# Performance work log

Hardware: AMD Instinct MI355X
Metric: run time of the kernel (lower is better)

The kernel has to match this reference:

```python
import jax, jax.numpy as jnp
import numpy as np

B, S, D, H, DH, RANK = 1, 2048, 1024, 16, 64, 16
NUM_ITERS = 5
EPS = 1e-6


def setup_inputs() -> dict:
    ks = jax.random.split(jax.random.key(0), 8)
    scale = 1.0 / np.sqrt(D)
    return {
        "x": jax.random.normal(ks[0], (B, S, D), dtype=jnp.float32),
        "Wq": jax.random.normal(ks[1], (D, D), dtype=jnp.float32) * scale,
        "Wk": jax.random.normal(ks[2], (D, D), dtype=jnp.float32) * scale,
        "Wv": jax.random.normal(ks[3], (D, D), dtype=jnp.float32) * scale,
        "Wo": jax.random.normal(ks[4], (D, D), dtype=jnp.float32) * scale,
        "bandwidth": jnp.array(1.0, dtype=jnp.float32),
        "diag_scale": jnp.ones((1, H, 1), dtype=jnp.float32),
        "pos_embedding": jax.random.normal(ks[5], (2048, RANK), dtype=jnp.float32) * 0.02,
        "head_proj": jax.random.normal(ks[6], (H, RANK, RANK), dtype=jnp.float32) * 0.02,
        "reg": jnp.array(0.1, dtype=jnp.float32),
        "lambda_reg": jnp.array(0.1, dtype=jnp.float32),
    }


def reference(x, Wq, Wk, Wv, Wo, bandwidth, diag_scale, pos_embedding, head_proj, reg, lambda_reg):
    b, s, d = x.shape
    h, dh = H, DH

    def heads(t):  # (b,s,d) -> (b,h,s,dh)
        return t.reshape(b, s, h, dh).transpose(0, 2, 1, 3)

    q = heads(x @ Wq)
    k = heads(x @ Wk)
    v = heads(x @ Wv)

    # RBF kernel via norm trick: ||q-k||^2 = ||q||^2 + ||k||^2 - 2 q.k
    bw = jax.nn.softplus(bandwidth) + EPS
    q_nsq = jnp.sum(q * q, axis=-1, keepdims=True)            # (b,h,s,1)
    k_nsq = jnp.sum(k * k, axis=-1, keepdims=True)            # (b,h,s,1)
    dist_sq = q_nsq + jnp.swapaxes(k_nsq, -2, -1) - 2.0 * jnp.einsum('bhsd,bhtd->bhst', q, k)
    dist_sq = jnp.maximum(dist_sq, 0.0)
    K = jnp.exp(-dist_sq / (2.0 * bw * bw))                   # (b,h,s,s)

    lam = jax.nn.softplus(lambda_reg)

    # Preconditioner P = diag(d) + U U^T
    kdiag = jnp.diagonal(K, axis1=-2, axis2=-1)               # (b,h,s)
    diag_p = jax.nn.softplus(kdiag) * diag_scale + reg        # (b,h,s)
    U = jnp.einsum('sr,hrp->hsp', pos_embedding[:s], head_proj)  # (h,s,rank)

    # Preconditioned Richardson iteration for (K + lam I) alpha = V
    alpha = jnp.zeros_like(v)
    for _ in range(NUM_ITERS):
        r = v - (jnp.einsum('bhst,bhtd->bhsd', K, alpha) + lam * alpha)
        ut_r = jnp.einsum('htr,bhtd->bhrd', U, r)
        p = r * diag_p[..., None] + jnp.einsum('hsr,bhrd->bhsd', U, ut_r)
        alpha = alpha + p

    out = jnp.einsum('bhst,bhtd->bhsd', K, alpha)             # output = K alpha
    out = out.transpose(0, 2, 1, 3).reshape(b, s, d) @ Wo
    return out
```

## Files before the change

### kernel.cpp

```cpp
#include <hip/hip_runtime.h>
#include <cstdint>
#include <cstddef>

constexpr int kS  = 2048;
constexpr int kD  = 1024;
constexpr int kH  = 16;
constexpr int kDH = 64;
constexpr int kR  = 16;

typedef __attribute__((ext_vector_type(8))) short bf16x8;
typedef __attribute__((ext_vector_type(4))) float f32x4;

__device__ __forceinline__ unsigned short kar_f2bf(float x) {
  unsigned u = __float_as_uint(x);
  return (unsigned short)((u + 0x7FFFu + ((u >> 16) & 1u)) >> 16);
}
__device__ __forceinline__ float kar_bf2f(short h) {
  return __uint_as_float((unsigned)(unsigned short)h << 16);
}
__device__ __forceinline__ void kar_split_bf(float x, short& hi, short& lo) {
  unsigned short h = kar_f2bf(x);
  float hf = __uint_as_float((unsigned)h << 16);
  hi = (short)h;
  lo = (short)kar_f2bf(x - hf);
}

__global__ __launch_bounds__(64) void kar_scalars_kernel(const float* __restrict__ bw,
                                                         const float* __restrict__ lreg,
                                                         double* __restrict__ SC) {
  if (threadIdx.x == 0) {
    double b = log1p(exp((double)bw[0])) + 1e-6;
    SC[0] = 1.0 / (2.0 * b * b);
    SC[1] = log1p(exp((double)lreg[0]));
  }
}

__global__ __launch_bounds__(256) void kar_u_kernel(const float* __restrict__ pe,
                                                    const float* __restrict__ hp,
                                                    float* __restrict__ U) {
  int o = blockIdx.x * 256 + threadIdx.x;
  int r = o & 15, s = (o >> 4) & 2047, h = o >> 15;
  double acc = 0.0;
#pragma unroll
  for (int rp = 0; rp < kR; rp++)
    acc += (double)pe[s * kR + rp] * (double)hp[((h * kR) + rp) * kR + r];
  U[o] = (float)acc;
}

__global__ __launch_bounds__(256) void kar_utr_partial_kernel(
    const float* __restrict__ Ubuf, const float* __restrict__ rbuf,
    double* __restrict__ utrp) {
  const int h  = blockIdx.y;
  const int sb = blockIdx.x * 64;
  const int t  = threadIdx.x;
  __shared__ float Uch[32][16];
  __shared__ float Rch[32][64];
  double acc[4] = {};
  for (int cs = 0; cs < 64; cs += 32) {
    __syncthreads();
    if (t < 128) {
      const int i = t >> 2, f = (t & 3) * 4;
      *(float4*)&Uch[i][f] = *(const float4*)&Ubuf[((size_t)(h * kS) + sb + cs + i) * kR + f];
    }
#pragma unroll
    for (int rep = 0; rep < 2; rep++) {
      const int e = t + rep * 256;
      const int i = e >> 4, c = (e & 15) * 4;
      *(float4*)&Rch[i][c] = *(const float4*)&rbuf[((size_t)(h * kS) + sb + cs + i) * kDH + c];
    }
    __syncthreads();
    for (int i = 0; i < 32; i++) {
#pragma unroll
      for (int rep = 0; rep < 4; rep++) {
        const int p = t + rep * 256;
        const int r = p >> 6, d = p & 63;
        acc[rep] += (double)Uch[i][r] * (double)Rch[i][d];
      }
    }
  }
#pragma unroll
  for (int rep = 0; rep < 4; rep++) {
    const int p = t + rep * 256;
    const int r = p >> 6, d = p & 63;
    utrp[(((size_t)(h * 32) + blockIdx.x) * kR + r) * kDH + d] = acc[rep];
  }
}

__global__ __launch_bounds__(256) void kar_utr_reduce_kernel(const double* __restrict__ utrp,
                                                             double* __restrict__ utr) {
  int o = blockIdx.x * 256 + threadIdx.x;
  int h = o >> 10, rd = o & 1023;
  double s = 0.0;
#pragma unroll
  for (int j = 0; j < 32; j++) s += utrp[(size_t)h * 32768 + (size_t)j * 1024 + rd];
  utr[o] = s;
}

__global__ __launch_bounds__(256) void kar_update_kernel(
    const float* __restrict__ rsrc, const double* __restrict__ dgp,
    const float* __restrict__ Ubuf, const double* __restrict__ utr,
    float* __restrict__ alpha, int first) {
  int e = blockIdx.x * 256 + threadIdx.x;
  const int d = e & 63;
  const int s = (e >> 6) & 2047;
  const int h = e >> 17;
  const double rv = (double)rsrc[e];
  const double dp = dgp[h * kS + s];
  const float*  Us = &Ubuf[((size_t)(h * kS) + s) * kR];
  const double* uh = &utr[(size_t)h * kR * kDH];
  double sum = 0.0;
#pragma unroll
  for (int ri = 0; ri < kR; ri++) sum += (double)Us[ri] * uh[ri * kDH + d];
  const double p = rv * dp + sum;
  const double an = (first ? 0.0 : (double)alpha[e]) + p;
  alpha[e] = (float)an;
}

__global__ __launch_bounds__(256) void kar_update_t_kernel(
    const float* __restrict__ rsrc, const double* __restrict__ dgp,
    const float* __restrict__ Ubuf, const double* __restrict__ utr,
    float* __restrict__ alpha, short* __restrict__ ath, int first) {
  const int h = blockIdx.y, s0 = blockIdx.x * 64;
  __shared__ float T[64][65];
  const int t = threadIdx.x;
  const int r16 = t >> 4, c4 = (t & 15) * 4;
  const double* uh = &utr[(size_t)h * kR * kDH];
#pragma unroll
  for (int it = 0; it < 4; it++) {
    const int row = it * 16 + r16;
    const int s = s0 + row;
    const size_t eg = ((size_t)h * kS + s) * kDH + c4;
    const float4 rv4 = *(const float4*)&rsrc[eg];
    const double dp = dgp[h * kS + s];
    const float* Us = &Ubuf[((size_t)h * kS + s) * kR];
    double sum0 = 0.0, sum1 = 0.0, sum2 = 0.0, sum3 = 0.0;
#pragma unroll
    for (int ri = 0; ri < kR; ri++) {
      const double u = (double)Us[ri];
      const double* ur = &uh[ri * kDH + c4];
      sum0 += u * ur[0]; sum1 += u * ur[1];
      sum2 += u * ur[2]; sum3 += u * ur[3];
    }
    double a0 = (first ? 0.0 : (double)alpha[eg + 0]) + ((double)rv4.x * dp + sum0);
    double a1 = (first ? 0.0 : (double)alpha[eg + 1]) + ((double)rv4.y * dp + sum1);
    double a2 = (first ? 0.0 : (double)alpha[eg + 2]) + ((double)rv4.z * dp + sum2);
    double a3 = (first ? 0.0 : (double)alpha[eg + 3]) + ((double)rv4.w * dp + sum3);
    float4 o;
    o.x = (float)a0; o.y = (float)a1; o.z = (float)a2; o.w = (float)a3;
    *(float4*)&alpha[eg] = o;
    T[row][c4] = o.x; T[row][c4 + 1] = o.y; T[row][c4 + 2] = o.z; T[row][c4 + 3] = o.w;
  }
  __syncthreads();
#pragma unroll
  for (int it = 0; it < 4; it++) {
    int d = it * 16 + r16;
    float v0 = T[c4][d], v1 = T[c4 + 1][d], v2 = T[c4 + 2][d], v3 = T[c4 + 3][d];
    *(short4*)&ath[((size_t)h * kDH + d) * kS + s0 + c4] =
        make_short4((short)kar_f2bf(v0), (short)kar_f2bf(v1),
                    (short)kar_f2bf(v2), (short)kar_f2bf(v3));
  }
}


__global__ __launch_bounds__(256) void kar_xsplit_kernel(const float* __restrict__ x,
                                                         short* __restrict__ xh,
                                                         short* __restrict__ xl) {
  size_t e = ((size_t)blockIdx.x * 256 + threadIdx.x) * 4;
  float4 a = *(const float4*)&x[e];
  short h0, l0, h1, l1, h2, l2, h3, l3;
  kar_split_bf(a.x, h0, l0); kar_split_bf(a.y, h1, l1);
  kar_split_bf(a.z, h2, l2); kar_split_bf(a.w, h3, l3);
  *(short4*)&xh[e] = make_short4(h0, h1, h2, h3);
  *(short4*)&xl[e] = make_short4(l0, l1, l2, l3);
}

__global__ __launch_bounds__(256) void kar_wsplit_kernel(
    const float* __restrict__ Wq, const float* __restrict__ Wk,
    const float* __restrict__ Wv, const float* __restrict__ Wo,
    short* __restrict__ WTh, short* __restrict__ WTl) {
  const float* W = (blockIdx.z == 0) ? Wq : (blockIdx.z == 1) ? Wk
                 : (blockIdx.z == 2) ? Wv : Wo;
  short* oh = WTh + (size_t)blockIdx.z * kD * kD;
  short* ol = WTl + (size_t)blockIdx.z * kD * kD;
  const int n0 = blockIdx.x * 64, k0 = blockIdx.y * 64;
  __shared__ float T[64][65];
  const int t = threadIdx.x;
  const int r16 = t >> 4, c4 = (t & 15) * 4;
#pragma unroll
  for (int it = 0; it < 4; it++) {
    int r = it * 16 + r16;
    float4 a = *(const float4*)&W[(size_t)(k0 + r) * kD + n0 + c4];
    T[r][c4] = a.x; T[r][c4 + 1] = a.y; T[r][c4 + 2] = a.z; T[r][c4 + 3] = a.w;
  }
  __syncthreads();
#pragma unroll
  for (int it = 0; it < 4; it++) {
    int n = it * 16 + r16;
    float v0 = T[c4][n], v1 = T[c4 + 1][n], v2 = T[c4 + 2][n], v3 = T[c4 + 3][n];
    short h0, l0, h1, l1, h2, l2, h3, l3;
    kar_split_bf(v0, h0, l0); kar_split_bf(v1, h1, l1);
    kar_split_bf(v2, h2, l2); kar_split_bf(v3, h3, l3);
    *(short4*)&oh[(size_t)(n0 + n) * kD + k0 + c4] = make_short4(h0, h1, h2, h3);
    *(short4*)&ol[(size_t)(n0 + n) * kD + k0 + c4] = make_short4(l0, l1, l2, l3);
  }
}

__global__ __launch_bounds__(256) void kar_mfma_gemm_qkv_kernel(
    const short* __restrict__ xh, const short* __restrict__ xl,
    const short* __restrict__ WTh, const short* __restrict__ WTl,
    float* __restrict__ v,
    short* __restrict__ qsh, short* __restrict__ qsl,
    short* __restrict__ ksh, short* __restrict__ ksl) {
  const int z = blockIdx.z;
  const short* Bh = WTh + (size_t)z * kD * kD;
  const short* Bl = WTl + (size_t)z * kD * kD;
  const int n0 = blockIdx.x * 64;
  const int m0 = blockIdx.y * 128;
  constexpr int LW = 40;
  __shared__ short Xh[128 * LW], Xl[128 * LW], Wh[64 * LW], Wl[64 * LW];
  const int t = threadIdx.x, lane = t & 63, wv = t >> 6;
  const int wm = wv >> 1, wn = wv & 1, l16 = lane & 15, qd = lane >> 4;
  f32x4 acc[4][2];
#pragma unroll
  for (int i = 0; i < 4; i++)
#pragma unroll
    for (int j = 0; j < 2; j++) acc[i][j] = (f32x4){0.f, 0.f, 0.f, 0.f};
  const int xrow = t >> 1, xc = (t & 1) * 16;
  for (int k0 = 0; k0 < kD; k0 += 32) {
    __syncthreads();
    {
      const size_t xs = (size_t)(m0 + xrow) * kD + k0 + xc;
      *(bf16x8*)&Xh[xrow * LW + xc]     = *(const bf16x8*)&xh[xs];
      *(bf16x8*)&Xh[xrow * LW + xc + 8] = *(const bf16x8*)&xh[xs + 8];
      *(bf16x8*)&Xl[xrow * LW + xc]     = *(const bf16x8*)&xl[xs];
      *(bf16x8*)&Xl[xrow * LW + xc + 8] = *(const bf16x8*)&xl[xs + 8];
    }
    if (t < 128) {
      const int wrow = t >> 1, wc = (t & 1) * 16;
      const size_t wsrc = (size_t)(n0 + wrow) * kD + k0 + wc;
      *(bf16x8*)&Wh[wrow * LW + wc]     = *(const bf16x8*)&Bh[wsrc];
      *(bf16x8*)&Wh[wrow * LW + wc + 8] = *(const bf16x8*)&Bh[wsrc + 8];
    } else {
      const int t2 = t - 128, wrow = t2 >> 1, wc = (t2 & 1) * 16;
      const size_t wsrc = (size_t)(n0 + wrow) * kD + k0 + wc;
      *(bf16x8*)&Wl[wrow * LW + wc]     = *(const bf16x8*)&Bl[wsrc];
      *(bf16x8*)&Wl[wrow * LW + wc + 8] = *(const bf16x8*)&Bl[wsrc + 8];
    }
    __syncthreads();
    bf16x8 bH[2], bL[2];
#pragma unroll
    for (int ni = 0; ni < 2; ni++) {
      const int rn = wn * 32 + ni * 16 + l16;
      bH[ni] = *(const bf16x8*)&Wh[rn * LW + qd * 8];
      bL[ni] = *(const bf16x8*)&Wl[rn * LW + qd * 8];
    }
#pragma unroll
    for (int mi = 0; mi < 4; mi++) {
      const int rm = wm * 64 + mi * 16 + l16;
      const bf16x8 aH = *(const bf16x8*)&Xh[rm * LW + qd * 8];
      const bf16x8 aL = *(const bf16x8*)&Xl[rm * LW + qd * 8];
#pragma unroll
      for (int ni = 0; ni < 2; ni++) {
        acc[mi][ni] = __builtin_amdgcn_mfma_f32_16x16x32_bf16(aH, bH[ni], acc[mi][ni], 0, 0, 0);
        acc[mi][ni] = __builtin_amdgcn_mfma_f32_16x16x32_bf16(aL, bH[ni], acc[mi][ni], 0, 0, 0);
        acc[mi][ni] = __builtin_amdgcn_mfma_f32_16x16x32_bf16(aH, bL[ni], acc[mi][ni], 0, 0, 0);
      }
    }
  }
  const int h = blockIdx.x;
#pragma unroll
  for (int mi = 0; mi < 4; mi++)
#pragma unroll
    for (int ni = 0; ni < 2; ni++) {
      const int d = wn * 32 + ni * 16 + l16;
#pragma unroll
      for (int r = 0; r < 4; r++) {
        const int s = m0 + wm * 64 + mi * 16 + qd * 4 + r;
        const float val = acc[mi][ni][r];
        const size_t idx = (((size_t)h * kS) + s) * kDH + d;
        if (z == 2) {
          v[idx] = val;
        } else {
          short hh, ll; kar_split_bf(val, hh, ll);
          if (z == 0) { qsh[idx] = hh; qsl[idx] = ll; }
          else        { ksh[idx] = hh; ksl[idx] = ll; }
        }
      }
    }
}

__global__ __launch_bounds__(256) void kar_mfma_gemm_wo_kernel(
    const short* __restrict__ th, const short* __restrict__ tl,
    const short* __restrict__ Bh, const short* __restrict__ Bl,
    float* __restrict__ outp) {
  const int n0 = blockIdx.x * 64;
  const int m0 = blockIdx.y * 128;
  constexpr int LW = 40;
  __shared__ short Xh[128 * LW], Xl[128 * LW], Wh[64 * LW], Wl[64 * LW];
  const int t = threadIdx.x, lane = t & 63, wv = t >> 6;
  const int wm = wv >> 1, wn = wv & 1, l16 = lane & 15, qd = lane >> 4;
  f32x4 acc[4][2];
#pragma unroll
  for (int i = 0; i < 4; i++)
#pragma unroll
    for (int j = 0; j < 2; j++) acc[i][j] = (f32x4){0.f, 0.f, 0.f, 0.f};
  const int xrow = t >> 1, xc = (t & 1) * 16;
  for (int k0 = 0; k0 < kD; k0 += 32) {
    __syncthreads();
    {
      const size_t xs = (size_t)(m0 + xrow) * kD + k0 + xc;
      *(bf16x8*)&Xh[xrow * LW + xc]     = *(const bf16x8*)&th[xs];
      *(bf16x8*)&Xh[xrow * LW + xc + 8] = *(const bf16x8*)&th[xs + 8];
      *(bf16x8*)&Xl[xrow * LW + xc]     = *(const bf16x8*)&tl[xs];
      *(bf16x8*)&Xl[xrow * LW + xc + 8] = *(const bf16x8*)&tl[xs + 8];
    }
    if (t < 128) {
      const int wrow = t >> 1, wc = (t & 1) * 16;
      const size_t wsrc = (size_t)(n0 + wrow) * kD + k0 + wc;
      *(bf16x8*)&Wh[wrow * LW + wc]     = *(const bf16x8*)&Bh[wsrc];
      *(bf16x8*)&Wh[wrow * LW + wc + 8] = *(const bf16x8*)&Bh[wsrc + 8];
    } else {
      const int t2 = t - 128, wrow = t2 >> 1, wc = (t2 & 1) * 16;
      const size_t wsrc = (size_t)(n0 + wrow) * kD + k0 + wc;
      *(bf16x8*)&Wl[wrow * LW + wc]     = *(const bf16x8*)&Bl[wsrc];
      *(bf16x8*)&Wl[wrow * LW + wc + 8] = *(const bf16x8*)&Bl[wsrc + 8];
    }
    __syncthreads();
    bf16x8 bH[2], bL[2];
#pragma unroll
    for (int ni = 0; ni < 2; ni++) {
      const int rn = wn * 32 + ni * 16 + l16;
      bH[ni] = *(const bf16x8*)&Wh[rn * LW + qd * 8];
      bL[ni] = *(const bf16x8*)&Wl[rn * LW + qd * 8];
    }
#pragma unroll
    for (int mi = 0; mi < 4; mi++) {
      const int rm = wm * 64 + mi * 16 + l16;
      const bf16x8 aH = *(const bf16x8*)&Xh[rm * LW + qd * 8];
      const bf16x8 aL = *(const bf16x8*)&Xl[rm * LW + qd * 8];
#pragma unroll
      for (int ni = 0; ni < 2; ni++) {
        acc[mi][ni] = __builtin_amdgcn_mfma_f32_16x16x32_bf16(aH, bH[ni], acc[mi][ni], 0, 0, 0);
        acc[mi][ni] = __builtin_amdgcn_mfma_f32_16x16x32_bf16(aL, bH[ni], acc[mi][ni], 0, 0, 0);
        acc[mi][ni] = __builtin_amdgcn_mfma_f32_16x16x32_bf16(aH, bL[ni], acc[mi][ni], 0, 0, 0);
      }
    }
  }
#pragma unroll
  for (int mi = 0; mi < 4; mi++)
#pragma unroll
    for (int ni = 0; ni < 2; ni++) {
      const int col = n0 + wn * 32 + ni * 16 + l16;
#pragma unroll
      for (int r = 0; r < 4; r++) {
        const int s = m0 + wm * 64 + mi * 16 + qd * 4 + r;
        outp[(size_t)s * kD + col] = acc[mi][ni][r];
      }
    }
}

__global__ __launch_bounds__(256) void kar_norms2_kernel(
    const short* __restrict__ qsh, const short* __restrict__ qsl,
    const short* __restrict__ ksh, const short* __restrict__ ksl,
    double* __restrict__ qn, double* __restrict__ kn) {
  int o = blockIdx.x * 256 + threadIdx.x;
  const short *sh, *sl; double* dst; int p;
  if (o < kH * kS) { sh = qsh; sl = qsl; dst = qn; p = o; }
  else             { sh = ksh; sl = ksl; dst = kn; p = o - kH * kS; }
  const short* rh = sh + (size_t)p * kDH;
  const short* rl = sl + (size_t)p * kDH;
  double s = 0.0;
  for (int i = 0; i < kDH; i += 4) {
    short4 a = *(const short4*)&rh[i];
    short4 b = *(const short4*)&rl[i];
    double e0 = (double)kar_bf2f(a.x) + (double)kar_bf2f(b.x);
    double e1 = (double)kar_bf2f(a.y) + (double)kar_bf2f(b.y);
    double e2 = (double)kar_bf2f(a.z) + (double)kar_bf2f(b.z);
    double e3 = (double)kar_bf2f(a.w) + (double)kar_bf2f(b.w);
    s += e0 * e0 + e1 * e1 + e2 * e2 + e3 * e3;
  }
  dst[p] = s;
}

__global__ __launch_bounds__(256) void kar_diagp2_kernel(
    const short* __restrict__ qsh, const short* __restrict__ qsl,
    const short* __restrict__ ksh, const short* __restrict__ ksl,
    const double* __restrict__ qn, const double* __restrict__ kn,
    const double* __restrict__ SC, const float* __restrict__ dsc,
    const float* __restrict__ reg, double* __restrict__ dgp) {
  int o = blockIdx.x * 256 + threadIdx.x;
  int h = o >> 11;
  const short* qh = qsh + (size_t)o * kDH;
  const short* ql = qsl + (size_t)o * kDH;
  const short* kh = ksh + (size_t)o * kDH;
  const short* kl = ksl + (size_t)o * kDH;
  double dot = 0.0;
  for (int i = 0; i < kDH; i++) {
    double qi = (double)kar_bf2f(qh[i]) + (double)kar_bf2f(ql[i]);
    double ki = (double)kar_bf2f(kh[i]) + (double)kar_bf2f(kl[i]);
    dot += qi * ki;
  }
  double dist = fmax(qn[o] + kn[o] - 2.0 * dot, 0.0);
  double Kss = exp(-dist * SC[0]);
  double sp  = log1p(exp(Kss));
  dgp[o] = sp * (double)dsc[h] + (double)reg[0];
}

template <bool FINAL>
__global__ __launch_bounds__(256, 2) void kar_mfma_iter6_kernel(
    const short* __restrict__ qsh, const short* __restrict__ qsl,
    const short* __restrict__ ksh, const short* __restrict__ ksl,
    const short* __restrict__ ath,
    const float* __restrict__ alpha, const float* __restrict__ v,
    const double* __restrict__ qn, const double* __restrict__ kn,
    const double* __restrict__ SC, float* __restrict__ outp,
    short* __restrict__ tmph, short* __restrict__ tmpl,
    const float* __restrict__ Ug, double* __restrict__ utrp) {
  constexpr int LDW = 72;
  __shared__ short Ph[2][64 * LDW];
  __shared__ float qns[64];
  __shared__ float Ub[64][16];
  const int h   = blockIdx.y;
  const int s0  = blockIdx.x * 64;
  const int tid = threadIdx.x;
  const int lane = tid & 63;
  const int wv   = tid >> 6;
  const int l16  = lane & 15;
  const int qd   = lane >> 4;
  bf16x8 qH[4][2], qL[4][2];
#pragma unroll
  for (int sq = 0; sq < 4; sq++) {
    const size_t qb = (((size_t)h * kS) + s0 + sq * 16 + l16) * kDH;
    qH[sq][0] = *(const bf16x8*)&qsh[qb + qd * 8];
    qH[sq][1] = *(const bf16x8*)&qsh[qb + 32 + qd * 8];
    qL[sq][0] = *(const bf16x8*)&qsl[qb + qd * 8];
    qL[sq][1] = *(const bf16x8*)&qsl[qb + 32 + qd * 8];
  }
  if (tid < 64) qns[tid] = (float)qn[h * kS + s0 + tid];
  if (!FINAL)
    *(float4*)&Ub[tid >> 2][(tid & 3) * 4] =
        *(const float4*)&Ug[((size_t)h * kS + s0 + (tid >> 2)) * kR + (tid & 3) * 4];
  __syncthreads();
  const float cc = (float)SC[0];
  f32x4 acco[4];
#pragma unroll
  for (int i = 0; i < 4; i++) acco[i] = (f32x4){0.f, 0.f, 0.f, 0.f};

  const short*  kRowH = &ksh[(((size_t)h * kS) + wv * 16 + l16) * kDH];
  const short*  kRowL = &ksl[(((size_t)h * kS) + wv * 16 + l16) * kDH];
  const short*  aRow  = &ath[((size_t)h * kDH + wv * 16 + l16) * kS];
  const double* knp   = &kn[h * kS + wv * 16 + l16];

  int buf = 0;
  for (int t0 = 0; t0 < kS; t0 += 64, buf ^= 1) {
    const size_t ko0 = (size_t)t0 * kDH + qd * 8;
    const bf16x8 kH0 = *(const bf16x8*)&kRowH[ko0];
    const bf16x8 kH1 = *(const bf16x8*)&kRowH[ko0 + 32];
    const bf16x8 kL0 = *(const bf16x8*)&kRowL[ko0];
    const bf16x8 kL1 = *(const bf16x8*)&kRowL[ko0 + 32];
    const bf16x8 aH0 = *(const bf16x8*)&aRow[t0 + qd * 8];
    const bf16x8 aH1 = *(const bf16x8*)&aRow[t0 + 32 + qd * 8];
    const float  knr = (float)knp[t0];
    f32x4 accp[4];
#pragma unroll
    for (int i = 0; i < 4; i++) accp[i] = (f32x4){0.f, 0.f, 0.f, 0.f};
#pragma unroll
    for (int sq = 0; sq < 4; sq++) {
      accp[sq] = __builtin_amdgcn_mfma_f32_16x16x32_bf16(qH[sq][0], kH0, accp[sq], 0, 0, 0);
      accp[sq] = __builtin_amdgcn_mfma_f32_16x16x32_bf16(qL[sq][0], kH0, accp[sq], 0, 0, 0);
      accp[sq] = __builtin_amdgcn_mfma_f32_16x16x32_bf16(qH[sq][0], kL0, accp[sq], 0, 0, 0);
    }
#pragma unroll
    for (int sq = 0; sq < 4; sq++) {
      accp[sq] = __builtin_amdgcn_mfma_f32_16x16x32_bf16(qH[sq][1], kH1, accp[sq], 0, 0, 0);
      accp[sq] = __builtin_amdgcn_mfma_f32_16x16x32_bf16(qL[sq][1], kH1, accp[sq], 0, 0, 0);
      accp[sq] = __builtin_amdgcn_mfma_f32_16x16x32_bf16(qH[sq][1], kL1, accp[sq], 0, 0, 0);
    }
#pragma unroll
    for (int sq = 0; sq < 4; sq++) {
#pragma unroll
      for (int r = 0; r < 4; r++) {
        const int srow = sq * 16 + qd * 4 + r;
        const float e2 = fmaf(2.0f, accp[sq][r], -(qns[srow] + knr));
        const float val = __expf(fminf(e2, 0.0f) * cc);
        Ph[buf][srow * LDW + wv * 16 + l16] = (short)kar_f2bf(val);
      }
    }
    __syncthreads();
#pragma unroll
    for (int sq = 0; sq < 4; sq++) {
      const bf16x8 pH0 = *(const bf16x8*)&Ph[buf][(sq * 16 + l16) * LDW + qd * 8];
      acco[sq] = __builtin_amdgcn_mfma_f32_16x16x32_bf16(pH0, aH0, acco[sq], 0, 0, 0);
      const bf16x8 pH1 = *(const bf16x8*)&Ph[buf][(sq * 16 + l16) * LDW + 32 + qd * 8];
      acco[sq] = __builtin_amdgcn_mfma_f32_16x16x32_bf16(pH1, aH1, acco[sq], 0, 0, 0);
    }
  }
  const int d = wv * 16 + l16;
  if (FINAL) {
#pragma unroll
    for (int sq = 0; sq < 4; sq++) {
#pragma unroll
      for (int r = 0; r < 4; r++) {
        const int s = s0 + sq * 16 + qd * 4 + r;
        short hh, ll; kar_split_bf(acco[sq][r], hh, ll);
        tmph[(size_t)s * kD + h * kDH + d] = hh;
        tmpl[(size_t)s * kD + h * kDH + d] = ll;
      }
    }
  } else {
    const float lamf = (float)SC[1];
    float rv[4][4];
#pragma unroll
    for (int sq = 0; sq < 4; sq++) {
#pragma unroll
      for (int r = 0; r < 4; r++) {
        const int s = s0 + sq * 16 + qd * 4 + r;
        const size_t eg = ((size_t)h * kS + s) * kDH + d;
        const float rr = v[eg] - (acco[sq][r] + lamf * alpha[eg]);
        rv[sq][r] = rr;
        outp[eg] = rr;
      }
    }
    double uacc[16];
#pragma unroll
    for (int ri = 0; ri < 16; ri++) uacc[ri] = 0.0;
#pragma unroll
    for (int sq = 0; sq < 4; sq++) {
#pragma unroll
      for (int r = 0; r < 4; r++) {
        const int sl = sq * 16 + qd * 4 + r;
        const double rval = (double)rv[sq][r];
        const float4 u0 = *(const float4*)&Ub[sl][0];
        const float4 u1 = *(const float4*)&Ub[sl][4];
        const float4 u2 = *(const float4*)&Ub[sl][8];
        const float4 u3 = *(const float4*)&Ub[sl][12];
        uacc[0]  += (double)u0.x * rval; uacc[1]  += (double)u0.y * rval;
        uacc[2]  += (double)u0.z * rval; uacc[3]  += (double)u0.w * rval;
        uacc[4]  += (double)u1.x * rval; uacc[5]  += (double)u1.y * rval;
        uacc[6]  += (double)u1.z * rval; uacc[7]  += (double)u1.w * rval;
        uacc[8]  += (double)u2.x * rval; uacc[9]  += (double)u2.y * rval;
        uacc[10] += (double)u2.z * rval; uacc[11] += (double)u2.w * rval;
        uacc[12] += (double)u3.x * rval; uacc[13] += (double)u3.y * rval;
        uacc[14] += (double)u3.z * rval; uacc[15] += (double)u3.w * rval;
      }
    }
#pragma unroll
    for (int ri = 0; ri < 16; ri++) {
      uacc[ri] += __shfl_xor(uacc[ri], 16, 64);
      uacc[ri] += __shfl_xor(uacc[ri], 32, 64);
    }
    if (qd == 0) {
#pragma unroll
      for (int ri = 0; ri < 16; ri++)
        utrp[(((size_t)(h * 32) + blockIdx.x) * kR + ri) * kDH + d] = uacc[ri];
    }
  }
}

__global__ __launch_bounds__(256) void kar_gemm_qkv_f32_kernel(
    const float* __restrict__ x,
    const float* __restrict__ Wq, const float* __restrict__ Wk, const float* __restrict__ Wv,
    float* __restrict__ q, float* __restrict__ k, float* __restrict__ v) {
  const float* W = (blockIdx.z == 0) ? Wq : (blockIdx.z == 1) ? Wk : Wv;
  float* outp    = (blockIdx.z == 0) ? q  : (blockIdx.z == 1) ? k  : v;
  const int n0 = blockIdx.x * 64;
  const int m0 = blockIdx.y * 64;
  const int tid = threadIdx.x;
  const int tx = tid & 15, ty = tid >> 4;
  __shared__ float As[16][68];
  __shared__ float Bs[16][68];
  double acc[4][4] = {};
  const int lr = tid >> 2;
  const int lk = (tid & 3) * 4;
  const int br = tid >> 4;
  const int bc = (tid & 15) * 4;
  for (int k0 = 0; k0 < kD; k0 += 16) {
    const float4 a4 = *(const float4*)&x[(size_t)(m0 + lr) * kD + k0 + lk];
    const float4 b4 = *(const float4*)&W[(size_t)(k0 + br) * kD + n0 + bc];
    __syncthreads();
    As[lk + 0][lr] = a4.x; As[lk + 1][lr] = a4.y;
    As[lk + 2][lr] = a4.z; As[lk + 3][lr] = a4.w;
    *(float4*)&Bs[br][bc] = b4;
    __syncthreads();
    float c32[4][4] = {};
#pragma unroll
    for (int kk = 0; kk < 16; kk++) {
      const float4 av = *(const float4*)&As[kk][ty * 4];
      const float4 bv = *(const float4*)&Bs[kk][tx * 4];
      const float a_[4] = {av.x, av.y, av.z, av.w};
      const float b_[4] = {bv.x, bv.y, bv.z, bv.w};
#pragma unroll
      for (int i = 0; i < 4; i++)
#pragma unroll
        for (int j = 0; j < 4; j++) c32[i][j] = fmaf(a_[i], b_[j], c32[i][j]);
    }
#pragma unroll
    for (int i = 0; i < 4; i++)
#pragma unroll
      for (int j = 0; j < 4; j++) acc[i][j] += (double)c32[i][j];
  }
  const int h = n0 >> 6;
#pragma unroll
  for (int i = 0; i < 4; i++) {
    const int s = m0 + ty * 4 + i;
    float4 o;
    o.x = (float)acc[i][0]; o.y = (float)acc[i][1];
    o.z = (float)acc[i][2]; o.w = (float)acc[i][3];
    *(float4*)&outp[((size_t)h * kS + s) * kDH + tx * 4] = o;
  }
}

__global__ __launch_bounds__(256) void kar_gemm_plain_kernel(
    const float* __restrict__ A, const float* __restrict__ W, float* __restrict__ C) {
  const int n0 = blockIdx.x * 64;
  const int m0 = blockIdx.y * 64;
  const int tid = threadIdx.x;
  const int tx = tid & 15, ty = tid >> 4;
  __shared__ float As[16][68];
  __shared__ float Bs[16][68];
  double acc[4][4] = {};
  const int lr = tid >> 2;
  const int lk = (tid & 3) * 4;
  const int br = tid >> 4;
  const int bc = (tid & 15) * 4;
  for (int k0 = 0; k0 < kD; k0 += 16) {
    const float4 a4 = *(const float4*)&A[(size_t)(m0 + lr) * kD + k0 + lk];
    const float4 b4 = *(const float4*)&W[(size_t)(k0 + br) * kD + n0 + bc];
    __syncthreads();
    As[lk + 0][lr] = a4.x; As[lk + 1][lr] = a4.y;
    As[lk + 2][lr] = a4.z; As[lk + 3][lr] = a4.w;
    *(float4*)&Bs[br][bc] = b4;
    __syncthreads();
    float c32[4][4] = {};
#pragma unroll
    for (int kk = 0; kk < 16; kk++) {
      const float4 av = *(const float4*)&As[kk][ty * 4];
      const float4 bv = *(const float4*)&Bs[kk][tx * 4];
      const float a_[4] = {av.x, av.y, av.z, av.w};
      const float b_[4] = {bv.x, bv.y, bv.z, bv.w};
#pragma unroll
      for (int i = 0; i < 4; i++)
#pragma unroll
        for (int j = 0; j < 4; j++) c32[i][j] = fmaf(a_[i], b_[j], c32[i][j]);
    }
#pragma unroll
    for (int i = 0; i < 4; i++)
#pragma unroll
      for (int j = 0; j < 4; j++) acc[i][j] += (double)c32[i][j];
  }
#pragma unroll
  for (int i = 0; i < 4; i++) {
    const int s = m0 + ty * 4 + i;
    float4 o;
    o.x = (float)acc[i][0]; o.y = (float)acc[i][1];
    o.z = (float)acc[i][2]; o.w = (float)acc[i][3];
    *(float4*)&C[(size_t)s * kD + n0 + tx * 4] = o;
  }
}

__global__ __launch_bounds__(256) void kar_norms_f32_kernel(const float* __restrict__ q,
                                                            const float* __restrict__ k,
                                                            double* __restrict__ qn,
                                                            double* __restrict__ kn) {
  int o = blockIdx.x * 256 + threadIdx.x;
  const float* src; double* dst; int p;
  if (o < kH * kS) { src = q; dst = qn; p = o; }
  else             { src = k; dst = kn; p = o - kH * kS; }
  const float* rowp = src + (size_t)p * kDH;
  double s = 0.0;
  for (int i = 0; i < kDH; i += 4) {
    float4 x4 = *(const float4*)&rowp[i];
    s += (double)x4.x * (double)x4.x + (double)x4.y * (double)x4.y +
         (double)x4.z * (double)x4.z + (double)x4.w * (double)x4.w;
  }
  dst[p] = s;
}

__global__ __launch_bounds__(256) void kar_diagp_f32_kernel(
    const float* __restrict__ q, const float* __restrict__ k,
    const double* __restrict__ qn, const double* __restrict__ kn,
    const double* __restrict__ SC, const float* __restrict__ dsc,
    const float* __restrict__ reg, double* __restrict__ dgp) {
  int o = blockIdx.x * 256 + threadIdx.x;
  int h = o >> 11;
  const float* qp = q + (size_t)o * kDH;
  const float* kp = k + (size_t)o * kDH;
  double dot = 0.0;
  for (int i = 0; i < kDH; i++) dot += (double)qp[i] * (double)kp[i];
  double dist = fmax(qn[o] + kn[o] - 2.0 * dot, 0.0);
  double Kss = exp(-dist * SC[0]);
  double sp  = log1p(exp(Kss));
  dgp[o] = sp * (double)dsc[h] + (double)reg[0];
}

template <bool FINAL>
__global__ __launch_bounds__(256, 2) void kar_mfma_iterA_kernel(
    const float* __restrict__ q, const float* __restrict__ k,
    const float* __restrict__ alpha, const float* __restrict__ v,
    const double* __restrict__ qn, const double* __restrict__ kn,
    const double* __restrict__ SC, float* __restrict__ outp) {
  constexpr int LDW = 72;
  __shared__ short Qh[64 * LDW], Ql[64 * LDW];
  __shared__ short Kh[64 * LDW], Kl[64 * LDW];
  __shared__ short Ph[64 * LDW], Pl[64 * LDW];
  __shared__ short Ah[64 * LDW], Al[64 * LDW];
  __shared__ float qns[64], kns[64];
  const int h   = blockIdx.y;
  const int s0  = blockIdx.x * 64;
  const int tid = threadIdx.x;
  const int lane = tid & 63;
  const int wv   = tid >> 6;
  const int l16  = lane & 15;
  const int qd   = lane >> 4;
  const int m16  = wv * 16;
  const float* qh = q + ((size_t)h * kS + s0) * kDH;
  const float* kh = k + (size_t)h * kS * kDH;
  const float* ah = alpha + (size_t)h * kS * kDH;
  {
    const int row = tid >> 4;
    const int c4  = (tid & 15) * 4;
#pragma unroll
    for (int rep = 0; rep < 4; rep++) {
      const int r = rep * 16 + row;
      const float4 a = *(const float4*)&qh[(size_t)r * kDH + c4];
      short h0, l0, h1, l1, h2, l2, h3, l3;
      kar_split_bf(a.x, h0, l0); kar_split_bf(a.y, h1, l1);
      kar_split_bf(a.z, h2, l2); kar_split_bf(a.w, h3, l3);
      *(short4*)&Qh[r * LDW + c4] = make_short4(h0, h1, h2, h3);
      *(short4*)&Ql[r * LDW + c4] = make_short4(l0, l1, l2, l3);
    }
    if (tid < 64) qns[tid] = (float)qn[h * kS + s0 + tid];
  }
  const float cc = (float)SC[0];
  f32x4 acco[4];
#pragma unroll
  for (int i = 0; i < 4; i++) acco[i] = (f32x4){0.f, 0.f, 0.f, 0.f};
  for (int t0 = 0; t0 < kS; t0 += 64) {
    __syncthreads();
    {
      const int row = tid >> 4;
      const int c4  = (tid & 15) * 4;
#pragma unroll
      for (int rep = 0; rep < 4; rep++) {
        const int r = rep * 16 + row;
        const float4 b = *(const float4*)&kh[(size_t)(t0 + r) * kDH + c4];
        short h0, l0, h1, l1, h2, l2, h3, l3;
        kar_split_bf(b.x, h0, l0); kar_split_bf(b.y, h1, l1);
        kar_split_bf(b.z, h2, l2); kar_split_bf(b.w, h3, l3);
        *(short4*)&Kh[r * LDW + c4] = make_short4(h0, h1, h2, h3);
        *(short4*)&Kl[r * LDW + c4] = make_short4(l0, l1, l2, l3);
        const float4 av = *(const float4*)&ah[(size_t)(t0 + r) * kDH + c4];
        kar_split_bf(av.x, h0, l0); kar_split_bf(av.y, h1, l1);
        kar_split_bf(av.z, h2, l2); kar_split_bf(av.w, h3, l3);
        Ah[(c4 + 0) * LDW + r] = h0; Al[(c4 + 0) * LDW + r] = l0;
        Ah[(c4 + 1) * LDW + r] = h1; Al[(c4 + 1) * LDW + r] = l1;
        Ah[(c4 + 2) * LDW + r] = h2; Al[(c4 + 2) * LDW + r] = l2;
        Ah[(c4 + 3) * LDW + r] = h3; Al[(c4 + 3) * LDW + r] = l3;
      }
      if (tid < 64) kns[tid] = (float)kn[h * kS + t0 + tid];
    }
    __syncthreads();
    f32x4 accp[4];
#pragma unroll
    for (int i = 0; i < 4; i++) accp[i] = (f32x4){0.f, 0.f, 0.f, 0.f};
#pragma unroll
    for (int kt = 0; kt < 2; kt++) {
      const int ko = kt * 32 + qd * 8;
      const bf16x8 aH = *(const bf16x8*)&Qh[(m16 + l16) * LDW + ko];
      const bf16x8 aL = *(const bf16x8*)&Ql[(m16 + l16) * LDW + ko];
#pragma unroll
      for (int nt = 0; nt < 4; nt++) {
        const bf16x8 bH = *(const bf16x8*)&Kh[(nt * 16 + l16) * LDW + ko];
        const bf16x8 bL = *(const bf16x8*)&Kl[(nt * 16 + l16) * LDW + ko];
        accp[nt] = __builtin_amdgcn_mfma_f32_16x16x32_bf16(aH, bH, accp[nt], 0, 0, 0);
        accp[nt] = __builtin_amdgcn_mfma_f32_16x16x32_bf16(aL, bH, accp[nt], 0, 0, 0);
        accp[nt] = __builtin_amdgcn_mfma_f32_16x16x32_bf16(aH, bL, accp[nt], 0, 0, 0);
      }
    }
#pragma unroll
    for (int nt = 0; nt < 4; nt++) {
      const int tcol = nt * 16 + l16;
      const float kv = kns[tcol];
#pragma unroll
      for (int r = 0; r < 4; r++) {
        const int srow = m16 + qd * 4 + r;
        const float e2 = fmaf(2.0f, accp[nt][r], -(qns[srow] + kv));
        const float val = __expf(fminf(e2, 0.0f) * cc);
        short hb, lb; kar_split_bf(val, hb, lb);
        Ph[srow * LDW + tcol] = hb;
        Pl[srow * LDW + tcol] = lb;
      }
    }
#pragma unroll
    for (int kt = 0; kt < 2; kt++) {
      const int ko = kt * 32 + qd * 8;
      const bf16x8 pH = *(const bf16x8*)&Ph[(m16 + l16) * LDW + ko];
      const bf16x8 pL = *(const bf16x8*)&Pl[(m16 + l16) * LDW + ko];
#pragma unroll
      for (int dt = 0; dt < 4; dt++) {
        const bf16x8 bH = *(const bf16x8*)&Ah[(dt * 16 + l16) * LDW + ko];
        const bf16x8 bL = *(const bf16x8*)&Al[(dt * 16 + l16) * LDW + ko];
        acco[dt] = __builtin_amdgcn_mfma_f32_16x16x32_bf16(pH, bH, acco[dt], 0, 0, 0);
        acco[dt] = __builtin_amdgcn_mfma_f32_16x16x32_bf16(pL, bH, acco[dt], 0, 0, 0);
        acco[dt] = __builtin_amdgcn_mfma_f32_16x16x32_bf16(pH, bL, acco[dt], 0, 0, 0);
      }
    }
  }
  if (FINAL) {
#pragma unroll
    for (int dt = 0; dt < 4; dt++) {
#pragma unroll
      for (int r = 0; r < 4; r++) {
        const int s = s0 + m16 + qd * 4 + r;
        const int d = dt * 16 + l16;
        outp[(size_t)s * kD + h * kDH + d] = acco[dt][r];
      }
    }
  } else {
    const float lamf = (float)SC[1];
#pragma unroll
    for (int dt = 0; dt < 4; dt++) {
#pragma unroll
      for (int r = 0; r < 4; r++) {
        const int s = s0 + m16 + qd * 4 + r;
        const int d = dt * 16 + l16;
        const size_t eg = ((size_t)h * kS + s) * kDH + d;
        outp[eg] = v[eg] - (acco[dt][r] + lamf * alpha[eg]);
      }
    }
  }
}

extern "C" void kernel_launch(void* const* d_in, const int* in_sizes, int n_in,
                              void* d_out, int out_size, void* d_ws, size_t ws_size,
                              hipStream_t stream) {
  (void)in_sizes; (void)n_in; (void)out_size;
  const float* x    = (const float*)d_in[0];
  const float* Wq   = (const float*)d_in[1];
  const float* Wk   = (const float*)d_in[2];
  const float* Wv   = (const float*)d_in[3];
  const float* Wo   = (const float*)d_in[4];
  const float* bw   = (const float*)d_in[5];
  const float* dsc  = (const float*)d_in[6];
  const float* pe   = (const float*)d_in[7];
  const float* hp   = (const float*)d_in[8];
  const float* reg  = (const float*)d_in[9];
  const float* lreg = (const float*)d_in[10];
  float* out = (float*)d_out;

  char* w = (char*)d_ws;
  size_t off = 0;
  auto take = [&](size_t bytes) -> void* {
    void* p = w + off;
    off += (bytes + 255) & ~(size_t)255;
    return p;
  };
  const size_t HSD = (size_t)kH * kS * kDH;

  float*  v_    = (float*)take(HSD * 4);
  float*  alpha = (float*)take(HSD * 4);
  float*  rbuf  = (float*)take(HSD * 4);
  short*  qsh   = (short*)take(HSD * 2);
  short*  qsl   = (short*)take(HSD * 2);
  short*  ksh   = (short*)take(HSD * 2);
  short*  ksl   = (short*)take(HSD * 2);
  short*  ath   = (short*)take(HSD * 2);
  short*  xh    = (short*)take((size_t)kS * kD * 2);
  short*  xl    = (short*)take((size_t)kS * kD * 2);
  short*  WTh   = (short*)take((size_t)4 * kD * kD * 2);
  short*  WTl   = (short*)take((size_t)4 * kD * kD * 2);
  double* qn    = (double*)take((size_t)kH * kS * 8);
  double* kn    = (double*)take((size_t)kH * kS * 8);
  double* dgp   = (double*)take((size_t)kH * kS * 8);
  float*  U     = (float*)take((size_t)kH * kS * kR * 4);
  double* utr   = (double*)take((size_t)kH * kR * kDH * 8);
  double* utrp  = (double*)take((size_t)kH * 32 * kR * kDH * 8);
  double* SC    = (double*)take(256);
  const size_t need_new = off;

  if (ws_size >= need_new) {
    kar_scalars_kernel<<<1, 64, 0, stream>>>(bw, lreg, SC);
    kar_xsplit_kernel<<<2048, 256, 0, stream>>>(x, xh, xl);
    kar_wsplit_kernel<<<dim3(16, 16, 4), 256, 0, stream>>>(Wq, Wk, Wv, Wo, WTh, WTl);
    kar_mfma_gemm_qkv_kernel<<<dim3(16, 16, 3), 256, 0, stream>>>(
        xh, xl, WTh, WTl, v_, qsh, qsl, ksh, ksl);
    kar_norms2_kernel<<<256, 256, 0, stream>>>(qsh, qsl, ksh, ksl, qn, kn);
    kar_u_kernel<<<2048, 256, 0, stream>>>(pe, hp, U);
    kar_diagp2_kernel<<<128, 256, 0, stream>>>(qsh, qsl, ksh, ksl, qn, kn, SC, dsc, reg, dgp);

    kar_utr_partial_kernel<<<dim3(32, kH), 256, 0, stream>>>(U, v_, utrp);
    kar_utr_reduce_kernel<<<64, 256, 0, stream>>>(utrp, utr);
    kar_update_t_kernel<<<dim3(32, kH), 256, 0, stream>>>(v_, dgp, U, utr, alpha, ath, 1);

    for (int it = 1; it < 5; it++) {
      kar_mfma_iter6_kernel<false><<<dim3(32, kH), 256, 0, stream>>>(
          qsh, qsl, ksh, ksl, ath, alpha, v_, qn, kn, SC, rbuf, nullptr, nullptr, U, utrp);
      kar_utr_reduce_kernel<<<64, 256, 0, stream>>>(utrp, utr);
      kar_update_t_kernel<<<dim3(32, kH), 256, 0, stream>>>(rbuf, dgp, U, utr, alpha, ath, 0);
    }

    kar_mfma_iter6_kernel<true><<<dim3(32, kH), 256, 0, stream>>>(
        qsh, qsl, ksh, ksl, ath, alpha, v_, qn, kn, SC, rbuf, xh, xl, U, utrp);
    kar_mfma_gemm_wo_kernel<<<dim3(16, 16), 256, 0, stream>>>(
        xh, xl, WTh + (size_t)3 * kD * kD, WTl + (size_t)3 * kD * kD, out);
  } else {
    size_t off2 = 0;
    auto take2 = [&](size_t bytes) -> void* {
      void* p = w + off2;
      off2 += (bytes + 255) & ~(size_t)255;
      return p;
    };
    float*  q2    = (float*)take2(HSD * 4);
    float*  k2    = (float*)take2(HSD * 4);
    float*  v2    = (float*)take2(HSD * 4);
    float*  al2   = (float*)take2(HSD * 4);
    float*  rb2   = (float*)take2(HSD * 4);
    float*  tmp2  = (float*)take2((size_t)kS * kD * 4);
    double* qn2   = (double*)take2((size_t)kH * kS * 8);
    double* kn2   = (double*)take2((size_t)kH * kS * 8);
    double* dgp2  = (double*)take2((size_t)kH * kS * 8);
    float*  U2    = (float*)take2((size_t)kH * kS * kR * 4);
    double* utr2  = (double*)take2((size_t)kH * kR * kDH * 8);
    double* utrp2 = (double*)take2((size_t)kH * 32 * kR * kDH * 8);
    double* SC2   = (double*)take2(256);

    kar_scalars_kernel<<<1, 64, 0, stream>>>(bw, lreg, SC2);
    kar_gemm_qkv_f32_kernel<<<dim3(16, 32, 3), 256, 0, stream>>>(x, Wq, Wk, Wv, q2, k2, v2);
    kar_norms_f32_kernel<<<256, 256, 0, stream>>>(q2, k2, qn2, kn2);
    kar_u_kernel<<<2048, 256, 0, stream>>>(pe, hp, U2);
    kar_diagp_f32_kernel<<<128, 256, 0, stream>>>(q2, k2, qn2, kn2, SC2, dsc, reg, dgp2);

    kar_utr_partial_kernel<<<dim3(32, kH), 256, 0, stream>>>(U2, v2, utrp2);
    kar_utr_reduce_kernel<<<64, 256, 0, stream>>>(utrp2, utr2);
    kar_update_kernel<<<8192, 256, 0, stream>>>(v2, dgp2, U2, utr2, al2, 1);

    for (int it = 1; it < 5; it++) {
      kar_mfma_iterA_kernel<false><<<dim3(32, kH), 256, 0, stream>>>(
          q2, k2, al2, v2, qn2, kn2, SC2, rb2);
      kar_utr_partial_kernel<<<dim3(32, kH), 256, 0, stream>>>(U2, rb2, utrp2);
      kar_utr_reduce_kernel<<<64, 256, 0, stream>>>(utrp2, utr2);
      kar_update_kernel<<<8192, 256, 0, stream>>>(rb2, dgp2, U2, utr2, al2, 0);
    }
    kar_mfma_iterA_kernel<true><<<dim3(32, kH), 256, 0, stream>>>(
        q2, k2, al2, v2, qn2, kn2, SC2, tmp2);
    kar_gemm_plain_kernel<<<dim3(16, 32), 256, 0, stream>>>(tmp2, Wo, out);
  }
}
```

Before: 607.4 us.

## Halve query tile to 32 rows, double grid, and prefetch next K/alpha tile

The fused RBF-matvec iteration kernel now handles 32 query rows per block instead of 64, launching 1024 blocks instead of 512 with a higher occupancy hint. K-tile and alpha-tile register loads are software-prefetched one tile ahead. The U^T r partial buffers and the reduction are widened to 64 partials to match. The aim is more parallelism and latency hiding on a 256-CU part, at the cost of reading K and alpha twice as often per query row and a longer reduction.

```diff
diff --git a/kernel.cpp b/kernel.cpp
--- a/kernel.cpp
+++ b/kernel.cpp
@@ -51,38 +51,35 @@
     const float* __restrict__ Ubuf, const float* __restrict__ rbuf,
     double* __restrict__ utrp) {
   const int h  = blockIdx.y;
-  const int sb = blockIdx.x * 64;
+  const int sb = blockIdx.x * 32;
   const int t  = threadIdx.x;
   __shared__ float Uch[32][16];
   __shared__ float Rch[32][64];
   double acc[4] = {};
-  for (int cs = 0; cs < 64; cs += 32) {
-    __syncthreads();
-    if (t < 128) {
-      const int i = t >> 2, f = (t & 3) * 4;
-      *(float4*)&Uch[i][f] = *(const float4*)&Ubuf[((size_t)(h * kS) + sb + cs + i) * kR + f];
-    }
-#pragma unroll
-    for (int rep = 0; rep < 2; rep++) {
-      const int e = t + rep * 256;
-      const int i = e >> 4, c = (e & 15) * 4;
-      *(float4*)&Rch[i][c] = *(const float4*)&rbuf[((size_t)(h * kS) + sb + cs + i) * kDH + c];
-    }
-    __syncthreads();
-    for (int i = 0; i < 32; i++) {
-#pragma unroll
-      for (int rep = 0; rep < 4; rep++) {
-        const int p = t + rep * 256;
-        const int r = p >> 6, d = p & 63;
-        acc[rep] += (double)Uch[i][r] * (double)Rch[i][d];
-      }
+  if (t < 128) {
+    const int i = t >> 2, f = (t & 3) * 4;
+    *(float4*)&Uch[i][f] = *(const float4*)&Ubuf[((size_t)(h * kS) + sb + i) * kR + f];
+  }
+#pragma unroll
+  for (int rep = 0; rep < 2; rep++) {
+    const int e = t + rep * 256;
+    const int i = e >> 4, c = (e & 15) * 4;
+    *(float4*)&Rch[i][c] = *(const float4*)&rbuf[((size_t)(h * kS) + sb + i) * kDH + c];
+  }
+  __syncthreads();
+  for (int i = 0; i < 32; i++) {
+#pragma unroll
+    for (int rep = 0; rep < 4; rep++) {
+      const int p = t + rep * 256;
+      const int r = p >> 6, d = p & 63;
+      acc[rep] += (double)Uch[i][r] * (double)Rch[i][d];
     }
   }
 #pragma unroll
   for (int rep = 0; rep < 4; rep++) {
     const int p = t + rep * 256;
     const int r = p >> 6, d = p & 63;
-    utrp[(((size_t)(h * 32) + blockIdx.x) * kR + r) * kDH + d] = acc[rep];
+    utrp[(((size_t)(h * 64) + blockIdx.x) * kR + r) * kDH + d] = acc[rep];
   }
 }
 
@@ -92,7 +89,7 @@
   int h = o >> 10, rd = o & 1023;
   double s = 0.0;
 #pragma unroll
-  for (int j = 0; j < 32; j++) s += utrp[(size_t)h * 32768 + (size_t)j * 1024 + rd];
+  for (int j = 0; j < 64; j++) s += utrp[(size_t)h * 65536 + (size_t)j * 1024 + rd];
   utr[o] = s;
 }
 
@@ -407,7 +404,7 @@
 }
 
 template <bool FINAL>
-__global__ __launch_bounds__(256, 2) void kar_mfma_iter6_kernel(
+__global__ __launch_bounds__(256, 4) void kar_mfma_iter7_kernel(
     const short* __restrict__ qsh, const short* __restrict__ qsl,
     const short* __restrict__ ksh, const short* __restrict__ ksl,
     const short* __restrict__ ath,
@@ -417,88 +414,96 @@
     short* __restrict__ tmph, short* __restrict__ tmpl,
     const float* __restrict__ Ug, double* __restrict__ utrp) {
   constexpr int LDW = 72;
-  __shared__ short Ph[2][64 * LDW];
-  __shared__ float qns[64];
-  __shared__ float Ub[64][16];
+  __shared__ short Ph[2][32 * LDW];
+  __shared__ float qns[32];
+  __shared__ float Ub[32][16];
   const int h   = blockIdx.y;
-  const int s0  = blockIdx.x * 64;
+  const int s0  = blockIdx.x * 32;
   const int tid = threadIdx.x;
   const int lane = tid & 63;
   const int wv   = tid >> 6;
   const int l16  = lane & 15;
   const int qd   = lane >> 4;
-  bf16x8 qH[4][2], qL[4][2];
-#pragma unroll
-  for (int sq = 0; sq < 4; sq++) {
+  bf16x8 qH[2][2], qL[2][2];
+#pragma unroll
+  for (int sq = 0; sq < 2; sq++) {
     const size_t qb = (((size_t)h * kS) + s0 + sq * 16 + l16) * kDH;
     qH[sq][0] = *(const bf16x8*)&qsh[qb + qd * 8];
     qH[sq][1] = *(const bf16x8*)&qsh[qb + 32 + qd * 8];
     qL[sq][0] = *(const bf16x8*)&qsl[qb + qd * 8];
     qL[sq][1] = *(const bf16x8*)&qsl[qb + 32 + qd * 8];
   }
-  if (tid < 64) qns[tid] = (float)qn[h * kS + s0 + tid];
-  if (!FINAL)
+  if (tid < 32) qns[tid] = (float)qn[h * kS + s0 + tid];
+  if (!FINAL && tid < 128)
     *(float4*)&Ub[tid >> 2][(tid & 3) * 4] =
         *(const float4*)&Ug[((size_t)h * kS + s0 + (tid >> 2)) * kR + (tid & 3) * 4];
   __syncthreads();
   const float cc = (float)SC[0];
-  f32x4 acco[4];
-#pragma unroll
-  for (int i = 0; i < 4; i++) acco[i] = (f32x4){0.f, 0.f, 0.f, 0.f};
+  f32x4 acco[2];
+#pragma unroll
+  for (int i = 0; i < 2; i++) acco[i] = (f32x4){0.f, 0.f, 0.f, 0.f};
 
   const short*  kRowH = &ksh[(((size_t)h * kS) + wv * 16 + l16) * kDH];
   const short*  kRowL = &ksl[(((size_t)h * kS) + wv * 16 + l16) * kDH];
   const short*  aRow  = &ath[((size_t)h * kDH + wv * 16 + l16) * kS];
   const double* knp   = &kn[h * kS + wv * 16 + l16];
 
+  bf16x8 kHc0 = *(const bf16x8*)&kRowH[qd * 8];
+  bf16x8 kHc1 = *(const bf16x8*)&kRowH[32 + qd * 8];
+  bf16x8 kLc0 = *(const bf16x8*)&kRowL[qd * 8];
+  bf16x8 kLc1 = *(const bf16x8*)&kRowL[32 + qd * 8];
+  bf16x8 aHc0 = *(const bf16x8*)&aRow[qd * 8];
+  bf16x8 aHc1 = *(const bf16x8*)&aRow[32 + qd * 8];
+  float  knc  = (float)knp[0];
+
   int buf = 0;
   for (int t0 = 0; t0 < kS; t0 += 64, buf ^= 1) {
-    const size_t ko0 = (size_t)t0 * kDH + qd * 8;
-    const bf16x8 kH0 = *(const bf16x8*)&kRowH[ko0];
-    const bf16x8 kH1 = *(const bf16x8*)&kRowH[ko0 + 32];
-    const bf16x8 kL0 = *(const bf16x8*)&kRowL[ko0];
-    const bf16x8 kL1 = *(const bf16x8*)&kRowL[ko0 + 32];
-    const bf16x8 aH0 = *(const bf16x8*)&aRow[t0 + qd * 8];
-    const bf16x8 aH1 = *(const bf16x8*)&aRow[t0 + 32 + qd * 8];
-    const float  knr = (float)knp[t0];
-    f32x4 accp[4];
-#pragma unroll
-    for (int i = 0; i < 4; i++) accp[i] = (f32x4){0.f, 0.f, 0.f, 0.f};
-#pragma unroll
-    for (int sq = 0; sq < 4; sq++) {
-      accp[sq] = __builtin_amdgcn_mfma_f32_16x16x32_bf16(qH[sq][0], kH0, accp[sq], 0, 0, 0);
-      accp[sq] = __builtin_amdgcn_mfma_f32_16x16x32_bf16(qL[sq][0], kH0, accp[sq], 0, 0, 0);
-      accp[sq] = __builtin_amdgcn_mfma_f32_16x16x32_bf16(qH[sq][0], kL0, accp[sq], 0, 0, 0);
-    }
-#pragma unroll
-    for (int sq = 0; sq < 4; sq++) {
-      accp[sq] = __builtin_amdgcn_mfma_f32_16x16x32_bf16(qH[sq][1], kH1, accp[sq], 0, 0, 0);
-      accp[sq] = __builtin_amdgcn_mfma_f32_16x16x32_bf16(qL[sq][1], kH1, accp[sq], 0, 0, 0);
-      accp[sq] = __builtin_amdgcn_mfma_f32_16x16x32_bf16(qH[sq][1], kL1, accp[sq], 0, 0, 0);
-    }
-#pragma unroll
-    for (int sq = 0; sq < 4; sq++) {
+    const int tn = (t0 + 64) & (kS - 1);
+    const size_t kon = (size_t)tn * kDH + qd * 8;
+    const bf16x8 kHn0 = *(const bf16x8*)&kRowH[kon];
+    const bf16x8 kHn1 = *(const bf16x8*)&kRowH[kon + 32];
+    const bf16x8 kLn0 = *(const bf16x8*)&kRowL[kon];
+    const bf16x8 kLn1 = *(const bf16x8*)&kRowL[kon + 32];
+    const bf16x8 aHn0 = *(const bf16x8*)&aRow[tn + qd * 8];
+    const bf16x8 aHn1 = *(const bf16x8*)&aRow[tn + 32 + qd * 8];
+    const float  knn  = (float)knp[tn];
+    f32x4 accp[2];
+#pragma unroll
+    for (int i = 0; i < 2; i++) accp[i] = (f32x4){0.f, 0.f, 0.f, 0.f};
+#pragma unroll
+    for (int sq = 0; sq < 2; sq++) {
+      accp[sq] = __builtin_amdgcn_mfma_f32_16x16x32_bf16(qH[sq][0], kHc0, accp[sq], 0, 0, 0);
+      accp[sq] = __builtin_amdgcn_mfma_f32_16x16x32_bf16(qL[sq][0], kHc0, accp[sq], 0, 0, 0);
+      accp[sq] = __builtin_amdgcn_mfma_f32_16x16x32_bf16(qH[sq][0], kLc0, accp[sq], 0, 0, 0);
+      accp[sq] = __builtin_amdgcn_mfma_f32_16x16x32_bf16(qH[sq][1], kHc1, accp[sq], 0, 0, 0);
+      accp[sq] = __builtin_amdgcn_mfma_f32_16x16x32_bf16(qL[sq][1], kHc1, accp[sq], 0, 0, 0);
+      accp[sq] = __builtin_amdgcn_mfma_f32_16x16x32_bf16(qH[sq][1], kLc1, accp[sq], 0, 0, 0);
+    }
+#pragma unroll
+    for (int sq = 0; sq < 2; sq++) {
 #pragma unroll
       for (int r = 0; r < 4; r++) {
         const int srow = sq * 16 + qd * 4 + r;
-        const float e2 = fmaf(2.0f, accp[sq][r], -(qns[srow] + knr));
+        const float e2 = fmaf(2.0f, accp[sq][r], -(qns[srow] + knc));
         const float val = __expf(fminf(e2, 0.0f) * cc);
         Ph[buf][srow * LDW + wv * 16 + l16] = (short)kar_f2bf(val);
       }
     }
     __syncthreads();
 #pragma unroll
-    for (int sq = 0; sq < 4; sq++) {
+    for (int sq = 0; sq < 2; sq++) {
       const bf16x8 pH0 = *(const bf16x8*)&Ph[buf][(sq * 16 + l16) * LDW + qd * 8];
-      acco[sq] = __builtin_amdgcn_mfma_f32_16x16x32_bf16(pH0, aH0, acco[sq], 0, 0, 0);
+      acco[sq] = __builtin_amdgcn_mfma_f32_16x16x32_bf16(pH0, aHc0, acco[sq], 0, 0, 0);
       const bf16x8 pH1 = *(const bf16x8*)&Ph[buf][(sq * 16 + l16) * LDW + 32 + qd * 8];
-      acco[sq] = __builtin_amdgcn_mfma_f32_16x16x32_bf16(pH1, aH1, acco[sq], 0, 0, 0);
-    }
+      acco[sq] = __builtin_amdgcn_mfma_f32_16x16x32_bf16(pH1, aHc1, acco[sq], 0, 0, 0);
+    }
+    kHc0 = kHn0; kHc1 = kHn1; kLc0 = kLn0; kLc1 = kLn1;
+    aHc0 = aHn0; aHc1 = aHn1; knc = knn;
   }
   const int d = wv * 16 + l16;
   if (FINAL) {
 #pragma unroll
-    for (int sq = 0; sq < 4; sq++) {
+    for (int sq = 0; sq < 2; sq++) {
 #pragma unroll
       for (int r = 0; r < 4; r++) {
         const int s = s0 + sq * 16 + qd * 4 + r;
@@ -509,9 +514,9 @@
     }
   } else {
     const float lamf = (float)SC[1];
-    float rv[4][4];
-#pragma unroll
-    for (int sq = 0; sq < 4; sq++) {
+    float rv[2][4];
+#pragma unroll
+    for (int sq = 0; sq < 2; sq++) {
 #pragma unroll
       for (int r = 0; r < 4; r++) {
         const int s = s0 + sq * 16 + qd * 4 + r;
@@ -525,7 +530,7 @@
 #pragma unroll
     for (int ri = 0; ri < 16; ri++) uacc[ri] = 0.0;
 #pragma unroll
-    for (int sq = 0; sq < 4; sq++) {
+    for (int sq = 0; sq < 2; sq++) {
 #pragma unroll
       for (int r = 0; r < 4; r++) {
         const int sl = sq * 16 + qd * 4 + r;
@@ -552,7 +557,7 @@
     if (qd == 0) {
 #pragma unroll
       for (int ri = 0; ri < 16; ri++)
-        utrp[(((size_t)(h * 32) + blockIdx.x) * kR + ri) * kDH + d] = uacc[ri];
+        utrp[(((size_t)(h * 64) + blockIdx.x) * kR + ri) * kDH + d] = uacc[ri];
     }
   }
 }
@@ -874,7 +879,7 @@
   double* dgp   = (double*)take((size_t)kH * kS * 8);
   float*  U     = (float*)take((size_t)kH * kS * kR * 4);
   double* utr   = (double*)take((size_t)kH * kR * kDH * 8);
-  double* utrp  = (double*)take((size_t)kH * 32 * kR * kDH * 8);
+  double* utrp  = (double*)take((size_t)kH * 64 * kR * kDH * 8);
   double* SC    = (double*)take(256);
   const size_t need_new = off;
 
@@ -888,18 +893,18 @@
     kar_u_kernel<<<2048, 256, 0, stream>>>(pe, hp, U);
     kar_diagp2_kernel<<<128, 256, 0, stream>>>(qsh, qsl, ksh, ksl, qn, kn, SC, dsc, reg, dgp);
 
-    kar_utr_partial_kernel<<<dim3(32, kH), 256, 0, stream>>>(U, v_, utrp);
+    kar_utr_partial_kernel<<<dim3(64, kH), 256, 0, stream>>>(U, v_, utrp);
     kar_utr_reduce_kernel<<<64, 256, 0, stream>>>(utrp, utr);
     kar_update_t_kernel<<<dim3(32, kH), 256, 0, stream>>>(v_, dgp, U, utr, alpha, ath, 1);
 
     for (int it = 1; it < 5; it++) {
-      kar_mfma_iter6_kernel<false><<<dim3(32, kH), 256, 0, stream>>>(
+      kar_mfma_iter7_kernel<false><<<dim3(64, kH), 256, 0, stream>>>(
           qsh, qsl, ksh, ksl, ath, alpha, v_, qn, kn, SC, rbuf, nullptr, nullptr, U, utrp);
       kar_utr_reduce_kernel<<<64, 256, 0, stream>>>(utrp, utr);
       kar_update_t_kernel<<<dim3(32, kH), 256, 0, stream>>>(rbuf, dgp, U, utr, alpha, ath, 0);
     }
 
-    kar_mfma_iter6_kernel<true><<<dim3(32, kH), 256, 0, stream>>>(
+    kar_mfma_iter7_kernel<true><<<dim3(64, kH), 256, 0, stream>>>(
         qsh, qsl, ksh, ksl, ath, alpha, v_, qn, kn, SC, rbuf, xh, xl, U, utrp);
     kar_mfma_gemm_wo_kernel<<<dim3(16, 16), 256, 0, stream>>>(
         xh, xl, WTh + (size_t)3 * kD * kD, WTl + (size_t)3 * kD * kD, out);
@@ -921,7 +926,7 @@
     double* dgp2  = (double*)take2((size_t)kH * kS * 8);
     float*  U2    = (float*)take2((size_t)kH * kS * kR * 4);
     double* utr2  = (double*)take2((size_t)kH * kR * kDH * 8);
-    double* utrp2 = (double*)take2((size_t)kH * 32 * kR * kDH * 8);
+    double* utrp2 = (double*)take2((size_t)kH * 64 * kR * kDH * 8);
     double* SC2   = (double*)take2(256);
 
     kar_scalars_kernel<<<1, 64, 0, stream>>>(bw, lreg, SC2);
@@ -930,14 +935,14 @@
     kar_u_kernel<<<2048, 256, 0, stream>>>(pe, hp, U2);
     kar_diagp_f32_kernel<<<128, 256, 0, stream>>>(q2, k2, qn2, kn2, SC2, dsc, reg, dgp2);
 
-    kar_utr_partial_kernel<<<dim3(32, kH), 256, 0, stream>>>(U2, v2, utrp2);
+    kar_utr_partial_kernel<<<dim3(64, kH), 256, 0, stream>>>(U2, v2, utrp2);
     kar_utr_reduce_kernel<<<64, 256, 0, stream>>>(utrp2, utr2);
     kar_update_kernel<<<8192, 256, 0, stream>>>(v2, dgp2, U2, utr2, al2, 1);
 
     for (int it = 1; it < 5; it++) {
       kar_mfma_iterA_kernel<false><<<dim3(32, kH), 256, 0, stream>>>(
           q2, k2, al2, v2, qn2, kn2, SC2, rb2);
-      kar_utr_partial_kernel<<<dim3(32, kH), 256, 0, stream>>>(U2, rb2, utrp2);
+      kar_utr_partial_kernel<<<dim3(64, kH), 256, 0, stream>>>(U2, rb2, utrp2);
       kar_utr_reduce_kernel<<<64, 256, 0, stream>>>(utrp2, utr2);
       kar_update_kernel<<<8192, 256, 0, stream>>>(rb2, dgp2, U2, utr2, al2, 0);
     }
```

Measured after the change: 799.4 us. 1.32x slower.
